# Performance work log

Measured on AMD Instinct MI355X. Metric: run time of the kernel, lower is better.

Reference implementation:

```python
import jax, jax.numpy as jnp
import numpy as np

N = 2_000_000
IN_CH = 10
UNITS = 32  # out_channels // 2 since last_vfe=False
KMAX = 64   # voxel coordinate range per axis


def setup_inputs() -> dict:
    key = jax.random.key(0)
    k1, k2, k3, k4, k5, k6, k7 = jax.random.split(key, 7)
    return {
        "inputs": jax.random.normal(k1, (N, IN_CH), dtype=jnp.float32),
        "mean": jax.random.normal(k2, (N, 6), dtype=jnp.float32),
        "linear_w": jax.random.normal(k3, (IN_CH, UNITS), dtype=jnp.float32) * 0.1,
        "linear_b": jax.random.normal(k4, (UNITS,), dtype=jnp.float32) * 0.1,
        "weight_w": jax.random.normal(k5, (6, UNITS), dtype=jnp.float32) * 0.1,
        "weight_b": jax.random.normal(k6, (UNITS,), dtype=jnp.float32) * 0.1,
        "bxyz_indx": jax.random.randint(k7, (N, 4), 0, KMAX, dtype=jnp.int32),
    }


def _encode_rows(bxyz_indx):
    # unique-by-row is equivalent to unique on a collision-free scalar key;
    # scatter_max-then-gather is invariant to how unique ids are labeled.
    b = bxyz_indx.astype(jnp.int64)
    return ((b[:, 0] * KMAX + b[:, 1]) * KMAX + b[:, 2]) * KMAX + b[:, 3]


def reference(inputs, mean, linear_w, linear_b, weight_w, weight_b, bxyz_indx):
    # x = relu(Linear(inputs)); gating by relu(Linear(mean))  (activate=True, gs=None)
    x = jax.nn.relu(inputs @ linear_w + linear_b)          # [N, UNITS]
    x_weight = jax.nn.relu(mean @ weight_w + weight_b)     # [N, UNITS]
    x = x * x_weight
    # unique voxel id per point -> inverse indices (jit-safe fixed size)
    keys = _encode_rows(bxyz_indx)
    _, inv = jnp.unique(keys, return_inverse=True, size=keys.shape[0], fill_value=-1)
    inv = inv.reshape(-1)
    # scatter_max over voxels, then gather back per point
    max_feature = jax.ops.segment_max(x, inv, num_segments=keys.shape[0])
    gather_max = max_feature[inv, :]                       # [N, UNITS]
    return jnp.concatenate([x, gather_max], axis=1)        # [N, 2*UNITS]
```

## Files before the change

### kernel.cpp

```cpp
#include <hip/hip_runtime.h>
#include <stdint.h>

#define IN_CH   10
#define MEAN_CH 6
#define UNITS   32
#define EMPTY_KEY ((int)0xAAAAAAAA)
#define KEYSPACE  (1 << 24)

typedef float f32x4 __attribute__((ext_vector_type(4)));

__global__ __launch_bounds__(256) void vfe_count(
    const int* __restrict__ bxyz, unsigned* __restrict__ cnt_words,
    int* __restrict__ keys, int nrows)
{
    int row = blockIdx.x * blockDim.x + threadIdx.x;
    if (row >= nrows) return;
    const int4 b = *(const int4*)(bxyz + (size_t)row * 4);
    int key = ((b.x * 64 + b.y) * 64 + b.z) * 64 + b.w;
    keys[row] = key;
    atomicAdd(&cnt_words[key >> 2], 1u << ((key & 3) * 8));
}

__global__ __launch_bounds__(256) void vfe_compute(
    const float* __restrict__ inputs, const float* __restrict__ mean,
    const float* __restrict__ W1, const float* __restrict__ b1,
    const float* __restrict__ W2, const float* __restrict__ b2,
    const int* __restrict__ keys, const unsigned char* __restrict__ cnt_bytes,
    int* __restrict__ ktab, int* __restrict__ slotidx,
    float* __restrict__ out, int* __restrict__ maxtab,
    unsigned cmask, int cshift, int nrows)
{
    int tid  = blockIdx.x * blockDim.x + threadIdx.x;
    int row  = tid >> 3;
    int lane8 = tid & 7;
    int c4   = lane8 * 4;
    if (row >= nrows) return;

    const float* __restrict__ in_row = inputs + (size_t)row * IN_CH;
    const float* __restrict__ mn_row = mean   + (size_t)row * MEAN_CH;

    float4 bb1 = *(const float4*)(b1 + c4);
    float a0 = bb1.x, a1 = bb1.y, a2 = bb1.z, a3 = bb1.w;
#pragma unroll
    for (int k = 0; k < IN_CH; ++k) {
        float v = in_row[k];
        float4 w = *(const float4*)(W1 + k * UNITS + c4);
        a0 = fmaf(v, w.x, a0); a1 = fmaf(v, w.y, a1);
        a2 = fmaf(v, w.z, a2); a3 = fmaf(v, w.w, a3);
    }
    a0 = fmaxf(a0, 0.0f); a1 = fmaxf(a1, 0.0f);
    a2 = fmaxf(a2, 0.0f); a3 = fmaxf(a3, 0.0f);

    float4 bb2 = *(const float4*)(b2 + c4);
    float g0 = bb2.x, g1 = bb2.y, g2 = bb2.z, g3 = bb2.w;
#pragma unroll
    for (int k = 0; k < MEAN_CH; ++k) {
        float v = mn_row[k];
        float4 w = *(const float4*)(W2 + k * UNITS + c4);
        g0 = fmaf(v, w.x, g0); g1 = fmaf(v, w.y, g1);
        g2 = fmaf(v, w.z, g2); g3 = fmaf(v, w.w, g3);
    }
    g0 = fmaxf(g0, 0.0f); g1 = fmaxf(g1, 0.0f);
    g2 = fmaxf(g2, 0.0f); g3 = fmaxf(g3, 0.0f);

    f32x4 x;
    x.x = a0 * g0; x.y = a1 * g1; x.z = a2 * g2; x.w = a3 * g3;

    *(f32x4*)(out + (size_t)row * 64 + c4)      = x;
    *(f32x4*)(out + (size_t)row * 64 + 32 + c4) = x;

    int key = keys[row];
    if (cnt_bytes[key] > 1) {
        int slot;
        if (lane8 == 0) {
            unsigned h = (((unsigned)key * 2654435761u) >> cshift) & cmask;
            while (true) {
                int old = atomicCAS(&ktab[h], EMPTY_KEY, key);
                if (old == EMPTY_KEY || old == key) break;
                h = (h + 1) & cmask;
            }
            slot = (int)h;
        }
        slot = __shfl(slot, 0, 8);
        int* __restrict__ mt = maxtab + (size_t)slot * UNITS + c4;
        atomicMax(mt + 0, (int)__float_as_uint(x.x));
        atomicMax(mt + 1, (int)__float_as_uint(x.y));
        atomicMax(mt + 2, (int)__float_as_uint(x.z));
        atomicMax(mt + 3, (int)__float_as_uint(x.w));
        if (lane8 == 0) slotidx[row] = slot;
    } else {
        if (lane8 == 0) slotidx[row] = -1;
    }
}

__global__ __launch_bounds__(256) void vfe_fixup(
    const int* __restrict__ slotidx, const int* __restrict__ maxtab,
    float* __restrict__ out, int nrows)
{
    int row = blockIdx.x * blockDim.x + threadIdx.x;
    if (row >= nrows) return;
    int s = slotidx[row];
    if (s < 0) return;
    const f32x4* src = (const f32x4*)(maxtab + (size_t)s * UNITS);
    f32x4* dst = (f32x4*)(out + (size_t)row * 64 + 32);
#pragma unroll
    for (int i = 0; i < 8; ++i) dst[i] = src[i];
}

extern "C" void kernel_launch(void* const* d_in, const int* in_sizes, int n_in,
                              void* d_out, int out_size, void* d_ws, size_t ws_size,
                              hipStream_t stream)
{
    const float* inputs = (const float*)d_in[0];
    const float* mean   = (const float*)d_in[1];
    const float* W1     = (const float*)d_in[2];
    const float* b1     = (const float*)d_in[3];
    const float* W2     = (const float*)d_in[4];
    const float* b2     = (const float*)d_in[5];
    const int*   bxyz   = (const int*)d_in[6];
    float* out = (float*)d_out;

    const int nrows = in_sizes[0] / IN_CH;

    unsigned cbits = 20;
    size_t need = (size_t)KEYSPACE
                + ((size_t)1 << cbits) * 4
                + (size_t)nrows * 4 * 2
                + ((size_t)1 << cbits) * UNITS * 4;
    if (need > ws_size) cbits = 19;
    const size_t CSIZE = (size_t)1 << cbits;
    const unsigned cmask = (unsigned)(CSIZE - 1);
    const int cshift = 32 - (int)cbits;

    char* p = (char*)d_ws;
    unsigned* cnt_words = (unsigned*)p;  p += KEYSPACE;
    int* ktab           = (int*)p;       p += CSIZE * 4;
    int* keys           = (int*)p;       p += (size_t)nrows * 4;
    int* slotidx        = (int*)p;       p += (size_t)nrows * 4;
    int* maxtab         = (int*)p;

    (void)hipMemsetAsync(cnt_words, 0, KEYSPACE, stream);
    (void)hipMemsetAsync(ktab, 0xAA, CSIZE * 4, stream);

    const int blk = 256;
    vfe_count<<<(nrows + blk - 1) / blk, blk, 0, stream>>>(
        bxyz, cnt_words, keys, nrows);

    const int total = nrows * 8;
    vfe_compute<<<(total + blk - 1) / blk, blk, 0, stream>>>(
        inputs, mean, W1, b1, W2, b2, keys, (const unsigned char*)cnt_words,
        ktab, slotidx, out, maxtab, cmask, cshift, nrows);

    vfe_fixup<<<(nrows + blk - 1) / blk, blk, 0, stream>>>(
        slotidx, maxtab, out, nrows);
}
```

Measured before the change: 931.7 us.

## Replace byte counters with seen/multi bitmaps and compact fixup worklist

Voxel occupancy counting now uses two bit-per-key bitmaps (seen and multi) instead of a byte-per-key count array. This shrinks the memset and counting footprint, and lets the hash table use zero as its empty tag so both can share one memset. The compute kernel skips writing the duplicate half for multi-point voxels and appends (row, slot) pairs to a compact worklist via an atomic counter. The fixup then processes only that list with a grid-stride loop instead of scanning every row. The cost is an extra global atomic counter per multi row and a worklist write whose order is nondeterministic.

```diff
diff --git a/kernel.cpp b/kernel.cpp
--- a/kernel.cpp
+++ b/kernel.cpp
@@ -4,37 +4,43 @@
 #define IN_CH   10
 #define MEAN_CH 6
 #define UNITS   32
-#define EMPTY_KEY ((int)0xAAAAAAAA)
-#define KEYSPACE  (1 << 24)
+#define KEYSPACE (1 << 24)
 
 typedef float f32x4 __attribute__((ext_vector_type(4)));
 
 __global__ __launch_bounds__(256) void vfe_count(
-    const int* __restrict__ bxyz, unsigned* __restrict__ cnt_words,
-    int* __restrict__ keys, int nrows)
+    const int* __restrict__ bxyz, unsigned* __restrict__ seen,
+    unsigned* __restrict__ multi, int* __restrict__ keys,
+    int* __restrict__ wcount, int nrows)
 {
     int row = blockIdx.x * blockDim.x + threadIdx.x;
+    if (row == 0) *wcount = 0;
     if (row >= nrows) return;
     const int4 b = *(const int4*)(bxyz + (size_t)row * 4);
     int key = ((b.x * 64 + b.y) * 64 + b.z) * 64 + b.w;
     keys[row] = key;
-    atomicAdd(&cnt_words[key >> 2], 1u << ((key & 3) * 8));
+    unsigned w = (unsigned)key >> 5, bit = 1u << (key & 31);
+    unsigned old = atomicOr(&seen[w], bit);
+    if (old & bit) atomicOr(&multi[w], bit);
 }
 
 __global__ __launch_bounds__(256) void vfe_compute(
     const float* __restrict__ inputs, const float* __restrict__ mean,
     const float* __restrict__ W1, const float* __restrict__ b1,
     const float* __restrict__ W2, const float* __restrict__ b2,
-    const int* __restrict__ keys, const unsigned char* __restrict__ cnt_bytes,
-    int* __restrict__ ktab, int* __restrict__ slotidx,
+    const int* __restrict__ keys, const unsigned* __restrict__ multi,
+    int* __restrict__ ktab, int* __restrict__ wcount, int2* __restrict__ wl,
     float* __restrict__ out, int* __restrict__ maxtab,
     unsigned cmask, int cshift, int nrows)
 {
-    int tid  = blockIdx.x * blockDim.x + threadIdx.x;
-    int row  = tid >> 3;
+    int tid   = blockIdx.x * blockDim.x + threadIdx.x;
+    int row   = tid >> 3;
     int lane8 = tid & 7;
-    int c4   = lane8 * 4;
+    int c4    = lane8 * 4;
     if (row >= nrows) return;
+
+    int key = keys[row];
+    bool is_multi = (multi[(unsigned)key >> 5] >> (key & 31)) & 1;
 
     const float* __restrict__ in_row = inputs + (size_t)row * IN_CH;
     const float* __restrict__ mn_row = mean   + (size_t)row * MEAN_CH;
@@ -66,20 +72,22 @@
     f32x4 x;
     x.x = a0 * g0; x.y = a1 * g1; x.z = a2 * g2; x.w = a3 * g3;
 
-    *(f32x4*)(out + (size_t)row * 64 + c4)      = x;
-    *(f32x4*)(out + (size_t)row * 64 + 32 + c4) = x;
-
-    int key = keys[row];
-    if (cnt_bytes[key] > 1) {
+    *(f32x4*)(out + (size_t)row * 64 + c4) = x;
+    if (!is_multi) {
+        *(f32x4*)(out + (size_t)row * 64 + 32 + c4) = x;
+    } else {
         int slot;
         if (lane8 == 0) {
             unsigned h = (((unsigned)key * 2654435761u) >> cshift) & cmask;
+            int tag = key + 1;
             while (true) {
-                int old = atomicCAS(&ktab[h], EMPTY_KEY, key);
-                if (old == EMPTY_KEY || old == key) break;
+                int old = atomicCAS(&ktab[h], 0, tag);
+                if (old == 0 || old == tag) break;
                 h = (h + 1) & cmask;
             }
             slot = (int)h;
+            int idx = atomicAdd(wcount, 1);
+            wl[idx] = make_int2(row, slot);
         }
         slot = __shfl(slot, 0, 8);
         int* __restrict__ mt = maxtab + (size_t)slot * UNITS + c4;
@@ -87,24 +95,22 @@
         atomicMax(mt + 1, (int)__float_as_uint(x.y));
         atomicMax(mt + 2, (int)__float_as_uint(x.z));
         atomicMax(mt + 3, (int)__float_as_uint(x.w));
-        if (lane8 == 0) slotidx[row] = slot;
-    } else {
-        if (lane8 == 0) slotidx[row] = -1;
     }
 }
 
 __global__ __launch_bounds__(256) void vfe_fixup(
-    const int* __restrict__ slotidx, const int* __restrict__ maxtab,
-    float* __restrict__ out, int nrows)
+    const int2* __restrict__ wl, const int* __restrict__ wcount,
+    const int* __restrict__ maxtab, float* __restrict__ out)
 {
-    int row = blockIdx.x * blockDim.x + threadIdx.x;
-    if (row >= nrows) return;
-    int s = slotidx[row];
-    if (s < 0) return;
-    const f32x4* src = (const f32x4*)(maxtab + (size_t)s * UNITS);
-    f32x4* dst = (f32x4*)(out + (size_t)row * 64 + 32);
-#pragma unroll
-    for (int i = 0; i < 8; ++i) dst[i] = src[i];
+    int n = *wcount;
+    int total = n * 8;
+    int stride = gridDim.x * blockDim.x;
+    for (int t = blockIdx.x * blockDim.x + threadIdx.x; t < total; t += stride) {
+        int i = t >> 3, l4 = (t & 7) * 4;
+        int2 e = wl[i];
+        f32x4 v = *(const f32x4*)(maxtab + (size_t)e.y * UNITS + l4);
+        *(f32x4*)(out + (size_t)e.x * 64 + 32 + l4) = v;
+    }
 }
 
 extern "C" void kernel_launch(void* const* d_in, const int* in_sizes, int n_in,
@@ -122,10 +128,13 @@
 
     const int nrows = in_sizes[0] / IN_CH;
 
+    const size_t BMWORDS = KEYSPACE / 32;
     unsigned cbits = 20;
-    size_t need = (size_t)KEYSPACE
+    size_t need = BMWORDS * 8
                 + ((size_t)1 << cbits) * 4
-                + (size_t)nrows * 4 * 2
+                + (size_t)nrows * 4
+                + 16
+                + (size_t)nrows * 8
                 + ((size_t)1 << cbits) * UNITS * 4;
     if (need > ws_size) cbits = 19;
     const size_t CSIZE = (size_t)1 << cbits;
@@ -133,24 +142,24 @@
     const int cshift = 32 - (int)cbits;
 
     char* p = (char*)d_ws;
-    unsigned* cnt_words = (unsigned*)p;  p += KEYSPACE;
-    int* ktab           = (int*)p;       p += CSIZE * 4;
-    int* keys           = (int*)p;       p += (size_t)nrows * 4;
-    int* slotidx        = (int*)p;       p += (size_t)nrows * 4;
-    int* maxtab         = (int*)p;
+    unsigned* seen  = (unsigned*)p;  p += BMWORDS * 4;
+    unsigned* multi = (unsigned*)p;  p += BMWORDS * 4;
+    int* ktab       = (int*)p;       p += CSIZE * 4;
+    int* keys       = (int*)p;       p += (size_t)nrows * 4;
+    int* wcount     = (int*)p;       p += 16;
+    int2* wl        = (int2*)p;      p += (size_t)nrows * 8;
+    int* maxtab     = (int*)p;
 
-    (void)hipMemsetAsync(cnt_words, 0, KEYSPACE, stream);
-    (void)hipMemsetAsync(ktab, 0xAA, CSIZE * 4, stream);
+    (void)hipMemsetAsync(seen, 0, BMWORDS * 8 + CSIZE * 4, stream);
 
     const int blk = 256;
     vfe_count<<<(nrows + blk - 1) / blk, blk, 0, stream>>>(
-        bxyz, cnt_words, keys, nrows);
+        bxyz, seen, multi, keys, wcount, nrows);
 
     const int total = nrows * 8;
     vfe_compute<<<(total + blk - 1) / blk, blk, 0, stream>>>(
-        inputs, mean, W1, b1, W2, b2, keys, (const unsigned char*)cnt_words,
-        ktab, slotidx, out, maxtab, cmask, cshift, nrows);
+        inputs, mean, W1, b1, W2, b2, keys, multi,
+        ktab, wcount, wl, out, maxtab, cmask, cshift, nrows);
 
-    vfe_fixup<<<(nrows + blk - 1) / blk, blk, 0, stream>>>(
-        slotidx, maxtab, out, nrows);
+    vfe_fixup<<<2048, blk, 0, stream>>>(wl, wcount, maxtab, out);
 }
```

After: 2.352 ms. +152.4%, slower.
